# Optimization experiments

Measured on AMD Instinct MI355X. Metric: run time of the kernel, lower is better.

## Reference

```python
import jax, jax.numpy as jnp
from jax import lax
import numpy as np

COST_CLASS, COST_BOX, COST_GIOU = 1.0, 5.0, 2.0
B, Q, C, T = 16, 900, 92, 100
INF = jnp.float32(1e18)


def setup_inputs() -> dict:
    key = jax.random.key(0)
    k1, k2, k3, k4 = jax.random.split(key, 4)
    pred_logits = jax.random.normal(k1, (B, Q, C), jnp.float32)

    def mk_boxes(k, n):
        kc, ks = jax.random.split(k)
        cxcy = jax.random.uniform(kc, (B, n, 2), jnp.float32) * 0.8 + 0.1
        wh = jax.random.uniform(ks, (B, n, 2), jnp.float32) * 0.2 + 0.05
        return jnp.concatenate([cxcy, wh], axis=-1)  # valid cxcywh in (0,1)

    pred_boxes = mk_boxes(k2, Q)
    tgt_boxes = mk_boxes(k3, T)
    tgt_labels = jax.random.randint(k4, (B, T), 0, C)
    return {"pred_logits": pred_logits, "pred_boxes": pred_boxes,
            "tgt_labels": tgt_labels, "tgt_boxes": tgt_boxes}


def box_cxcywh_to_xyxy(b):
    cx, cy, w, h = b[..., 0], b[..., 1], b[..., 2], b[..., 3]
    return jnp.stack([cx - 0.5 * w, cy - 0.5 * h, cx + 0.5 * w, cy + 0.5 * h], axis=-1)


def generalized_box_iou(a, b):
    # a: [B,Q,4] xyxy, b: [B,T,4] xyxy -> [B,Q,T]
    area_a = (a[..., 2] - a[..., 0]) * (a[..., 3] - a[..., 1])  # [B,Q]
    area_b = (b[..., 2] - b[..., 0]) * (b[..., 3] - b[..., 1])  # [B,T]
    a_ = a[:, :, None, :]
    b_ = b[:, None, :, :]
    lt = jnp.maximum(a_[..., :2], b_[..., :2])
    rb = jnp.minimum(a_[..., 2:], b_[..., 2:])
    wh = jnp.clip(rb - lt, 0.0)
    inter = wh[..., 0] * wh[..., 1]
    union = area_a[:, :, None] + area_b[:, None, :] - inter
    iou = inter / union
    lt_c = jnp.minimum(a_[..., :2], b_[..., :2])
    rb_c = jnp.maximum(a_[..., 2:], b_[..., 2:])
    wh_c = jnp.clip(rb_c - lt_c, 0.0)
    area_c = wh_c[..., 0] * wh_c[..., 1]
    return iou - (area_c - union) / area_c


def cost_matrix(pred_logits, pred_boxes, tgt_labels, tgt_boxes):
    probs = jax.nn.softmax(pred_logits, axis=-1)                         # [B,Q,C]
    cost_class = -jnp.take_along_axis(probs, tgt_labels[:, None, :], 2)  # [B,Q,T]
    cost_box = jnp.abs(pred_boxes[:, :, None, :] - tgt_boxes[:, None, :, :]).sum(-1)
    cost_giou = -generalized_box_iou(box_cxcywh_to_xyxy(pred_boxes),
                                     box_cxcywh_to_xyxy(tgt_boxes))
    return COST_BOX * cost_box + COST_CLASS * cost_class + COST_GIOU * cost_giou


def hungarian(cost):
    # Jonker-Volgenant shortest augmenting path. cost: [n, m], n <= m, minimize.
    # Returns col_for_row [n]: column assigned to each row.
    n, m = cost.shape

    def solve_row(i, uvp):
        u, v, p = uvp  # u:[n+1] row potentials, v:[m+1] col potentials, p:[m+1] col->row (n = free)
        p = p.at[m].set(i)  # virtual start column holds current row
        minv = jnp.full((m,), INF, jnp.float32)
        way = jnp.zeros((m,), jnp.int32)
        used = jnp.zeros((m + 1,), bool)
        j0 = jnp.int32(m)

        def cond(s):
            _, _, _, _, _, j0 = s
            return p[j0] != n  # stop when a free column is reached

        def body(s):
            u, v, minv, way, used, j0 = s
            used = used.at[j0].set(True)
            i0 = p[j0]
            cur = cost[i0] - u[i0] - v[:m]           # reduced costs of row i0
            mask = (~used[:m]) & (cur < minv)
            minv = jnp.where(mask, cur, minv)
            way = jnp.where(mask, j0, way)
            mvals = jnp.where(used[:m], INF, minv)
            j1 = jnp.argmin(mvals).astype(jnp.int32)
            delta = mvals[j1]
            u = u.at[p].add(jnp.where(used, delta, 0.0))
            v = v - jnp.where(used, delta, 0.0)
            minv = jnp.where(used[:m], minv, minv - delta)
            return (u, v, minv, way, used, j1)

        u, v, minv, way, used, j0 = lax.while_loop(cond, body, (u, v, minv, way, used, j0))

        def acond(s):
            _, j0 = s
            return j0 != m

        def abody(s):
            p, j0 = s
            j1 = way[j0]
            p = p.at[j0].set(p[j1])
            return (p, j1)

        p, _ = lax.while_loop(acond, abody, (p, j0))
        return (u, v, p)

    u0 = jnp.zeros((n + 1,), jnp.float32)
    v0 = jnp.zeros((m + 1,), jnp.float32)
    p0 = jnp.full((m + 1,), n, jnp.int32)
    _, _, p = lax.fori_loop(0, n, solve_row, (u0, v0, p0))
    col_for_row = jnp.zeros((n + 1,), jnp.int32).at[p[:m]].set(
        jnp.arange(m, dtype=jnp.int32))[:n]
    return col_for_row


def reference(pred_logits, pred_boxes, tgt_labels, tgt_boxes):
    cost = cost_matrix(pred_logits, pred_boxes, tgt_labels, tgt_boxes)  # [B,Q,T]
    # assign each target (row) to a distinct query (col); vmap over batch
    q_per_t = jax.vmap(hungarian)(jnp.swapaxes(cost, 1, 2))  # [B,T]
    order = jnp.argsort(q_per_t, axis=-1)                    # sort by query idx (scipy convention)
    q_idx = jnp.take_along_axis(q_per_t, order, axis=-1)     # query indices  [B,T]
    t_idx = order.astype(jnp.int32)                          # target indices [B,T]
    return cost, q_idx, t_idx
```

## Files before the change

### kernel.cpp

```cpp
#include <hip/hip_runtime.h>

#define BB 16
#define QQ 900
#define QP 960
#define VIRT QP
#define CC 92
#define TT 100
#define INFF 1e18f
#define NK 15

#define DPP_STEP_F(x, ctrl, OP)                                             \
  do {                                                                      \
    float _o = __int_as_float(__builtin_amdgcn_update_dpp(                  \
        __float_as_int(x), __float_as_int(x), (ctrl), 0xF, 0xF, false));    \
    (x) = OP((x), _o);                                                      \
  } while (0)

__device__ __forceinline__ float wave_fmax63(float x) {
  DPP_STEP_F(x, 0xB1, fmaxf);
  DPP_STEP_F(x, 0x4E, fmaxf);
  DPP_STEP_F(x, 0x141, fmaxf);
  DPP_STEP_F(x, 0x140, fmaxf);
  DPP_STEP_F(x, 0x142, fmaxf);
  DPP_STEP_F(x, 0x143, fmaxf);
  return x;
}
__device__ __forceinline__ float wave_fmin63(float x) {
  DPP_STEP_F(x, 0xB1, fminf);
  DPP_STEP_F(x, 0x4E, fminf);
  DPP_STEP_F(x, 0x141, fminf);
  DPP_STEP_F(x, 0x140, fminf);
  DPP_STEP_F(x, 0x142, fminf);
  DPP_STEP_F(x, 0x143, fminf);
  return x;
}
__device__ __forceinline__ float wave_fadd63(float x) {
#define ADDF(a, b) ((a) + (b))
  DPP_STEP_F(x, 0xB1, ADDF);
  DPP_STEP_F(x, 0x4E, ADDF);
  DPP_STEP_F(x, 0x141, ADDF);
  DPP_STEP_F(x, 0x140, ADDF);
  DPP_STEP_F(x, 0x142, ADDF);
  DPP_STEP_F(x, 0x143, ADDF);
#undef ADDF
  return x;
}
__device__ __forceinline__ int wave_imin63(int x) {
  {int _o=__builtin_amdgcn_update_dpp(x,x,0xB1,0xF,0xF,false); x=_o<x?_o:x;}
  {int _o=__builtin_amdgcn_update_dpp(x,x,0x4E,0xF,0xF,false); x=_o<x?_o:x;}
  {int _o=__builtin_amdgcn_update_dpp(x,x,0x141,0xF,0xF,false);x=_o<x?_o:x;}
  {int _o=__builtin_amdgcn_update_dpp(x,x,0x140,0xF,0xF,false);x=_o<x?_o:x;}
  {int _o=__builtin_amdgcn_update_dpp(x,x,0x142,0xF,0xF,false);x=_o<x?_o:x;}
  {int _o=__builtin_amdgcn_update_dpp(x,x,0x143,0xF,0xF,false);x=_o<x?_o:x;}
  return x;
}

__device__ __forceinline__ int p_get(unsigned a, unsigned b, unsigned c,
                                     unsigned d, int j) {
  const int l = j & 63, kq = j >> 6;
  unsigned r0 = (unsigned)__builtin_amdgcn_readlane((int)a, l);
  unsigned r1 = (unsigned)__builtin_amdgcn_readlane((int)b, l);
  unsigned r2 = (unsigned)__builtin_amdgcn_readlane((int)c, l);
  unsigned r3 = (unsigned)__builtin_amdgcn_readlane((int)d, l);
  unsigned r = (kq < 8) ? (kq < 4 ? r0 : r1) : (kq < 12 ? r2 : r3);
  return (int)((r >> ((kq & 3) * 8)) & 0xFFu);
}

#define P_SET(jj, val)                                                      \
  do {                                                                      \
    const int _j = (jj); const int _kq = _j >> 6;                           \
    const unsigned _sh = (unsigned)((_kq & 3) * 8);                         \
    const unsigned _nm = ~(0xFFu << _sh);                                   \
    const unsigned _in = ((unsigned)(val) & 0xFFu) << _sh;                  \
    const bool _own = (lane == (_j & 63));                                  \
    if (_kq < 4)       { if (_own) p4a = (p4a & _nm) | _in; }               \
    else if (_kq < 8)  { if (_own) p4b = (p4b & _nm) | _in; }               \
    else if (_kq < 12) { if (_own) p4c = (p4c & _nm) | _in; }               \
    else               { if (_own) p4d = (p4d & _nm) | _in; }               \
  } while (0)

__global__ __launch_bounds__(64) void cost_kernel(
    const float* __restrict__ logits,
    const float* __restrict__ pboxes,
    const int*   __restrict__ tlabels,
    const float* __restrict__ tboxes,
    float* __restrict__ cost,
    float* __restrict__ costT,
    int ctp)
{
  const int bq   = blockIdx.x;
  const int b    = bq / QQ;
  const int q    = bq - b * QQ;
  const int lane = threadIdx.x;

  __shared__ float sl[CC];

  const float a = logits[(size_t)bq * CC + lane];
  const float bb2 = (lane < CC - 64)
                        ? logits[(size_t)bq * CC + 64 + lane]
                        : -3.402823466e38f;

  float mx = fmaxf(a, bb2);
  mx = wave_fmax63(mx);
  const float m = __int_as_float(
      __builtin_amdgcn_readlane(__float_as_int(mx), 63));

  const float e0 = expf(a - m);
  const float e1 = (lane < CC - 64) ? expf(bb2 - m) : 0.0f;
  sl[lane] = e0;
  if (lane < CC - 64) sl[64 + lane] = e1;

  float sm = e0 + e1;
  sm = wave_fadd63(sm);
  const float ssum = __int_as_float(
      __builtin_amdgcn_readlane(__float_as_int(sm), 63));

  const float4 pbv = ((const float4*)pboxes)[bq];
  const float pax1 = pbv.x - 0.5f * pbv.z, pay1 = pbv.y - 0.5f * pbv.w;
  const float pax2 = pbv.x + 0.5f * pbv.z, pay2 = pbv.y + 0.5f * pbv.w;
  const float area_a = (pax2 - pax1) * (pay2 - pay1);

  for (int t = lane; t < TT; t += 64) {
    const int lab = tlabels[b * TT + t];
    const float cc = -(sl[lab] / ssum);

    const float4 tb = ((const float4*)tboxes)[b * TT + t];
    const float cbox = fabsf(pbv.x - tb.x) + fabsf(pbv.y - tb.y) +
                       fabsf(pbv.z - tb.z) + fabsf(pbv.w - tb.w);

    const float bx1 = tb.x - 0.5f * tb.z, by1 = tb.y - 0.5f * tb.w;
    const float bx2 = tb.x + 0.5f * tb.z, by2 = tb.y + 0.5f * tb.w;
    const float area_b = (bx2 - bx1) * (by2 - by1);

    const float ltx = fmaxf(pax1, bx1), lty = fmaxf(pay1, by1);
    const float rbx = fminf(pax2, bx2), rby = fminf(pay2, by2);
    const float iw = fmaxf(rbx - ltx, 0.0f), ih = fmaxf(rby - lty, 0.0f);
    const float inter = iw * ih;
    const float uni = area_a + area_b - inter;
    const float iou = inter / uni;

    const float cx1 = fminf(pax1, bx1), cy1 = fminf(pay1, by1);
    const float cx2 = fmaxf(pax2, bx2), cy2 = fmaxf(pay2, by2);
    const float cw = fmaxf(cx2 - cx1, 0.0f), ch = fmaxf(cy2 - cy1, 0.0f);
    const float ac = cw * ch;
    const float giou = iou - (ac - uni) / ac;

    const float cval = 5.0f * cbox + cc - 2.0f * giou;
    cost[(size_t)bq * TT + t] = cval;
    if (ctp) costT[((size_t)b * TT + t) * ctp + q] = cval;
  }
  if (ctp == QP && q < QP - QQ) {
    for (int t = lane; t < TT; t += 64)
      costT[((size_t)b * TT + t) * QP + QQ + q] = INFF;
  }
}

__global__ void __launch_bounds__(64)
hungarianT_kernel(
    const float* __restrict__ ct,
    float* __restrict__ out_q,
    float* __restrict__ out_t)
{
  const int b    = blockIdx.x;
  const int lane = threadIdx.x;

  __shared__ int way_lds[QP];
  __shared__ int qpt[TT];

  const float* __restrict__ base = ct + (size_t)b * TT * QP;

#pragma unroll
  for (int k = 0; k < NK; ++k) way_lds[k * 64 + lane] = -1;

  unsigned p4a = 0x64646464u, p4b = 0x64646464u;
  unsigned p4c = 0x64646464u, p4d = 0x64646464u;

  float u0 = 0.0f, u1 = 0.0f;
  float v[NK];
#pragma unroll
  for (int k = 0; k < NK; ++k) v[k] = 0.0f;

  float c[NK];
#pragma unroll
  for (int k = 0; k < NK; ++k) c[k] = base[k * 64 + lane];

  for (int i = 0; i < TT; ++i) {
    float minv[NK];
#pragma unroll
    for (int k = 0; k < NK; ++k) minv[k] = INFF;
    unsigned umask = 0;
    const int stamp = i << 12;

    int i0 = i;
    int j0 = VIRT;
    int jfin;

    float us = (i0 < 64) ? u0 : u1;
    float ui0 = __int_as_float(
        __builtin_amdgcn_readlane(__float_as_int(us), i0 & 63));

    for (int step = 0; step < 128; ++step) {
      const bool first = (j0 == VIRT);
      if (i0 == lane)      umask |= (1u << 30);
      if (i0 == 64 + lane) umask |= (1u << 31);
      if (!first && (j0 & 63) == lane) umask |= (1u << (j0 >> 6));

      float lmin  = INFF;
      int   kbest = 0;
#pragma unroll
      for (int k = 0; k < NK; ++k) {
        const bool  uk  = (umask >> k) & 1u;
        const float cur = c[k] - ui0 - v[k];
        const bool  imp = !uk && (cur < minv[k]);
        if (imp) {
          minv[k] = cur;
          if (!first) way_lds[k * 64 + lane] = stamp | j0;
        }
        const float eff = uk ? INFF : minv[k];
        if (eff < lmin) { lmin = eff; kbest = k; }
      }
      const int lidx = (kbest << 6) + lane;

      if (first && i + 1 < TT) {
        const float* __restrict__ nrow = base + (size_t)(i + 1) * QP;
#pragma unroll
        for (int k = 0; k < NK; ++k) c[k] = nrow[k * 64 + lane];
      }

      float red = wave_fmin63(lmin);
      const float delta = __int_as_float(
          __builtin_amdgcn_readlane(__float_as_int(red), 63));
      const unsigned long long bmask = __ballot(lmin == delta);
      const int wl = (int)(__ffsll((long long)bmask) - 1);
      const int j1 = __builtin_amdgcn_readlane(lidx, wl);

      const int  i0n = p_get(p4a, p4b, p4c, p4d, j1);
      const bool fin = (i0n == TT);

      if (!fin) {
        const float* __restrict__ prow = base + (size_t)i0n * QP;
#pragma unroll
        for (int k = 0; k < NK; ++k) c[k] = prow[k * 64 + lane];
      }

      u0 += ((umask >> 30) & 1u) ? delta : 0.0f;
      u1 += (umask >> 31)        ? delta : 0.0f;
#pragma unroll
      for (int k = 0; k < NK; ++k)
        v[k] -= ((umask >> k) & 1u) ? delta : 0.0f;
      if (!fin) {
#pragma unroll
        for (int k = 0; k < NK; ++k)
          minv[k] -= ((umask >> k) & 1u) ? 0.0f : delta;
      }
      asm volatile("" ::: "memory");

      if (fin) { jfin = j1; break; }
      float us2 = (i0n < 64) ? u0 : u1;
      ui0 = __int_as_float(
          __builtin_amdgcn_readlane(__float_as_int(us2), i0n & 63));
      j0 = j1;
      i0 = i0n;
    }

    const bool single = (j0 == VIRT);

    if (!single && i + 1 < TT) {
      const float* __restrict__ nrow = base + (size_t)(i + 1) * QP;
#pragma unroll
      for (int k = 0; k < NK; ++k) c[k] = nrow[k * 64 + lane];
    }

    if (single) {
      P_SET(jfin, i);
    } else {
      int j = jfin;
      for (int hop = 0; hop < 128 && j != VIRT; ++hop) {
        int raw = way_lds[j];
        raw = __builtin_amdgcn_readfirstlane(raw);
        const int jn = ((raw >> 12) == i) ? (raw & 0xFFF) : VIRT;
        const int pj = (jn == VIRT) ? i : p_get(p4a, p4b, p4c, p4d, jn);
        P_SET(j, pj);
        j = jn;
      }
    }
    asm volatile("" ::: "memory");
  }

#pragma unroll
  for (int k = 0; k < NK; ++k) {
    const unsigned reg = (k < 4) ? p4a : (k < 8) ? p4b : (k < 12) ? p4c : p4d;
    const int r = (int)((reg >> ((k & 3) * 8)) & 0xFFu);
    const int j = k * 64 + lane;
    if (r < TT) qpt[r] = j;
  }
  __syncthreads();

  for (int t = lane; t < TT; t += 64) {
    const int myq = qpt[t];
    int rank = 0;
    for (int t2 = 0; t2 < TT; ++t2) rank += (qpt[t2] < myq) ? 1 : 0;
    out_q[b * TT + rank] = (float)myq;
    out_t[b * TT + rank] = (float)t;
  }
}

__global__ void __launch_bounds__(64)
hungarian_kernel(
    const float* __restrict__ cost,
    const float* __restrict__ costT,
    float* __restrict__ out_q,
    float* __restrict__ out_t)
{
  const int b    = blockIdx.x;
  const int lane = threadIdx.x;

  __shared__ int p_lds[QQ + 1];
  __shared__ int way_lds[QQ];
  __shared__ int qpt[TT];

  const float* base;
  size_t rs, cs;
  if (costT) { base = costT + (size_t)b * TT * QQ; rs = QQ; cs = 1; }
  else       { base = cost  + (size_t)b * QQ * TT; rs = 1;  cs = TT; }

  for (int j = lane; j <= QQ; j += 64) p_lds[j] = TT;

  float u0 = 0.0f, u1 = 0.0f;
  float v[NK];
#pragma unroll
  for (int k = 0; k < NK; ++k) v[k] = 0.0f;

  float c[NK];
#pragma unroll
  for (int k = 0; k < NK; ++k) {
    const int j = k * 64 + lane;
    c[k] = (j < QQ) ? base[(size_t)j * cs] : 0.0f;
  }

  for (int i = 0; i < TT; ++i) {
    p_lds[QQ] = i;

    float minv[NK];
#pragma unroll
    for (int k = 0; k < NK; ++k) minv[k] = INFF;
    unsigned umask = 0;
    bool t0 = false, t1 = false;

    int i0 = i;
    int j0 = QQ;
    int jfin;

    float us = (i0 < 64) ? u0 : u1;
    float ui0 = __int_as_float(
        __builtin_amdgcn_readlane(__float_as_int(us), i0 & 63));

    while (true) {
      t0 = t0 || (i0 == lane);
      t1 = t1 || (i0 == 64 + lane);
      if (j0 != QQ) {
        if ((j0 & 63) == lane) umask |= (1u << (j0 >> 6));
      }

      float lmin = INFF;
      int   lidx = QQ;
#pragma unroll
      for (int k = 0; k < NK; ++k) {
        const int j = k * 64 + lane;
        if (j < QQ && !((umask >> k) & 1u)) {
          const float cur = c[k] - ui0 - v[k];
          if (cur < minv[k]) { minv[k] = cur; way_lds[j] = j0; }
          if (minv[k] < lmin) { lmin = minv[k]; lidx = j; }
        }
      }

      float red = wave_fmin63(lmin);
      const float delta = __int_as_float(
          __builtin_amdgcn_readlane(__float_as_int(red), 63));
      int cand = (lmin == delta) ? lidx : 0x7FFFFFFF;
      int redi = wave_imin63(cand);
      const int j1 = __builtin_amdgcn_readlane(redi, 63);

      int i0n = p_lds[j1];
      i0n = __builtin_amdgcn_readfirstlane(i0n);
      const bool fin = (i0n == TT);

      u0 += t0 ? delta : 0.0f;
      u1 += t1 ? delta : 0.0f;
#pragma unroll
      for (int k = 0; k < NK; ++k) {
        const bool uk = (umask >> k) & 1u;
        v[k]    -= uk ? delta : 0.0f;
        minv[k] -= uk ? 0.0f  : delta;
      }

      if (!fin) {
        float us2 = (i0n < 64) ? u0 : u1;
        ui0 = __int_as_float(
            __builtin_amdgcn_readlane(__float_as_int(us2), i0n & 63));
#pragma unroll
        for (int k = 0; k < NK; ++k) {
          const int j = k * 64 + lane;
          if (j < QQ) c[k] = base[(size_t)i0n * rs + (size_t)j * cs];
        }
      }
      asm volatile("" ::: "memory");

      if (fin) { jfin = j1; break; }
      j0 = j1;
      i0 = i0n;
    }

    if (i + 1 < TT) {
#pragma unroll
      for (int k = 0; k < NK; ++k) {
        const int jj = k * 64 + lane;
        if (jj < QQ) c[k] = base[(size_t)(i + 1) * rs + (size_t)jj * cs];
      }
    }

    int j = jfin;
    while (j != QQ) {
      const int jn = way_lds[j];
      const int pj = p_lds[jn];
      p_lds[j] = pj;
      j = jn;
    }
    asm volatile("" ::: "memory");
  }

#pragma unroll
  for (int k = 0; k < NK; ++k) {
    const int j = k * 64 + lane;
    if (j < QQ) {
      const int r = p_lds[j];
      if (r < TT) qpt[r] = j;
    }
  }
  __syncthreads();

  for (int t = lane; t < TT; t += 64) {
    const int myq = qpt[t];
    int rank = 0;
    for (int t2 = 0; t2 < TT; ++t2) rank += (qpt[t2] < myq) ? 1 : 0;
    out_q[b * TT + rank] = (float)myq;
    out_t[b * TT + rank] = (float)t;
  }
}

extern "C" void kernel_launch(void* const* d_in, const int* in_sizes, int n_in,
                              void* d_out, int out_size, void* d_ws, size_t ws_size,
                              hipStream_t stream) {
  const float* logits  = (const float*)d_in[0];
  const float* pboxes  = (const float*)d_in[1];
  const int*   tlabels = (const int*)d_in[2];
  const float* tboxes  = (const float*)d_in[3];

  float* out  = (float*)d_out;
  float* cost = out;
  float* oq   = out + (size_t)BB * QQ * TT;
  float* ot   = oq + (size_t)BB * TT;

  const size_t padded_bytes = (size_t)BB * TT * QP * sizeof(float);
  const size_t plain_bytes  = (size_t)BB * TT * QQ * sizeof(float);

  if (ws_size >= padded_bytes) {
    float* costT = (float*)d_ws;
    hipLaunchKernelGGL(cost_kernel, dim3(BB * QQ), dim3(64), 0, stream,
                       logits, pboxes, tlabels, tboxes, cost, costT, QP);
    hipLaunchKernelGGL(hungarianT_kernel, dim3(BB), dim3(64), 0, stream,
                       costT, oq, ot);
  } else if (ws_size >= plain_bytes) {
    float* costT = (float*)d_ws;
    hipLaunchKernelGGL(cost_kernel, dim3(BB * QQ), dim3(64), 0, stream,
                       logits, pboxes, tlabels, tboxes, cost, costT, QQ);
    hipLaunchKernelGGL(hungarian_kernel, dim3(BB), dim3(64), 0, stream,
                       cost, costT, oq, ot);
  } else {
    hipLaunchKernelGGL(cost_kernel, dim3(BB * QQ), dim3(64), 0, stream,
                       logits, pboxes, tlabels, tboxes, cost, (float*)nullptr, 0);
    hipLaunchKernelGGL(hungarian_kernel, dim3(BB), dim3(64), 0, stream,
                       cost, (const float*)nullptr, oq, ot);
  }
}
```

Baseline: 200.2 us.

## Batch single-step Hungarian rows speculatively, fall back on first column collision

Restructures the Hungarian solver into epochs. Each epoch precomputes each remaining row's minimum reduced-cost column without data dependencies, so row loads can be prefetched. It then commits rows in order whose chosen column is still free, and falls back to the full augmenting-path search only at the first collision. This is meant to cut the serial dependent-step latency for the many rows that augment in one step. The cost is that rows after a collision are recomputed in later epochs, which could do extra work when collisions happen early and often.

Result: slower. 247.8 us (+23.8%).

```diff
diff --git a/kernel.cpp b/kernel.cpp
--- a/kernel.cpp
+++ b/kernel.cpp
@@ -53,6 +53,10 @@
   {int _o=__builtin_amdgcn_update_dpp(x,x,0x142,0xF,0xF,false);x=_o<x?_o:x;}
   {int _o=__builtin_amdgcn_update_dpp(x,x,0x143,0xF,0xF,false);x=_o<x?_o:x;}
   return x;
+}
+
+__device__ __forceinline__ float readlane_f(float x, int l) {
+  return __int_as_float(__builtin_amdgcn_readlane(__float_as_int(x), l));
 }
 
 __device__ __forceinline__ int p_get(unsigned a, unsigned b, unsigned c,
@@ -102,8 +106,7 @@
 
   float mx = fmaxf(a, bb2);
   mx = wave_fmax63(mx);
-  const float m = __int_as_float(
-      __builtin_amdgcn_readlane(__float_as_int(mx), 63));
+  const float m = readlane_f(mx, 63);
 
   const float e0 = expf(a - m);
   const float e1 = (lane < CC - 64) ? expf(bb2 - m) : 0.0f;
@@ -112,8 +115,7 @@
 
   float sm = e0 + e1;
   sm = wave_fadd63(sm);
-  const float ssum = __int_as_float(
-      __builtin_amdgcn_readlane(__float_as_int(sm), 63));
+  const float ssum = readlane_f(sm, 63);
 
   const float4 pbv = ((const float4*)pboxes)[bq];
   const float pax1 = pbv.x - 0.5f * pbv.z, pay1 = pbv.y - 0.5f * pbv.w;
@@ -180,111 +182,149 @@
 #pragma unroll
   for (int k = 0; k < NK; ++k) v[k] = 0.0f;
 
-  float c[NK];
-#pragma unroll
-  for (int k = 0; k < NK; ++k) c[k] = base[k * 64 + lane];
-
-  for (int i = 0; i < TT; ++i) {
-    float minv[NK];
-#pragma unroll
-    for (int k = 0; k < NK; ++k) minv[k] = INFF;
-    unsigned umask = 0;
-    const int stamp = i << 12;
-
-    int i0 = i;
-    int j0 = VIRT;
-    int jfin;
-
-    float us = (i0 < 64) ? u0 : u1;
-    float ui0 = __int_as_float(
-        __builtin_amdgcn_readlane(__float_as_int(us), i0 & 63));
-
-    for (int step = 0; step < 128; ++step) {
-      const bool first = (j0 == VIRT);
-      if (i0 == lane)      umask |= (1u << 30);
-      if (i0 == 64 + lane) umask |= (1u << 31);
-      if (!first && (j0 & 63) == lane) umask |= (1u << (j0 >> 6));
-
+  int rbase = 0;
+  for (int epoch = 0; epoch <= TT && rbase < TT; ++epoch) {
+    float valv0 = 0.0f, valv1 = 0.0f;
+    int   colv0 = 0,    colv1 = 0;
+
+    float cn[NK];
+    {
+      const float* __restrict__ rp = base + (size_t)rbase * QP;
+#pragma unroll
+      for (int k = 0; k < NK; ++k) cn[k] = rp[k * 64 + lane];
+    }
+    for (int s = rbase; s < TT; ++s) {
+      float cc[NK];
+#pragma unroll
+      for (int k = 0; k < NK; ++k) cc[k] = cn[k];
+      if (s + 1 < TT) {
+        const float* __restrict__ rp = base + (size_t)(s + 1) * QP;
+#pragma unroll
+        for (int k = 0; k < NK; ++k) cn[k] = rp[k * 64 + lane];
+      }
       float lmin  = INFF;
       int   kbest = 0;
 #pragma unroll
       for (int k = 0; k < NK; ++k) {
-        const bool  uk  = (umask >> k) & 1u;
-        const float cur = c[k] - ui0 - v[k];
-        const bool  imp = !uk && (cur < minv[k]);
-        if (imp) {
-          minv[k] = cur;
-          if (!first) way_lds[k * 64 + lane] = stamp | j0;
+        const float cur = cc[k] - v[k];
+        if (cur < lmin) { lmin = cur; kbest = k; }
+      }
+      const int lidx = (kbest << 6) + lane;
+      float red = wave_fmin63(lmin);
+      const float delta = readlane_f(red, 63);
+      const unsigned long long bm = __ballot(lmin == delta);
+      const int wl = (int)(__ffsll((long long)bm) - 1);
+      const int j1 = __builtin_amdgcn_readlane(lidx, wl);
+      const int off = s - rbase;
+      if (off < 64) { if (lane == off)      { valv0 = delta; colv0 = j1; } }
+      else          { if (lane == off - 64) { valv1 = delta; colv1 = j1; } }
+    }
+
+    int sfb = -1;
+    for (int s = rbase; s < TT; ++s) {
+      const int off = s - rbase;
+      float sv; int sc;
+      if (off < 64) { sv = readlane_f(valv0, off);      sc = __builtin_amdgcn_readlane(colv0, off); }
+      else          { sv = readlane_f(valv1, off - 64); sc = __builtin_amdgcn_readlane(colv1, off - 64); }
+      const int pm = p_get(p4a, p4b, p4c, p4d, sc);
+      if (pm != TT) { sfb = s; break; }
+      P_SET(sc, s);
+      u0 = (lane == s)      ? sv : u0;
+      u1 = (lane == s - 64) ? sv : u1;
+    }
+    if (sfb < 0) { rbase = TT; break; }
+
+    {
+      const int s = sfb;
+      float c2[NK];
+      {
+        const float* __restrict__ rp = base + (size_t)s * QP;
+#pragma unroll
+        for (int k = 0; k < NK; ++k) c2[k] = rp[k * 64 + lane];
+      }
+      float minv[NK];
+#pragma unroll
+      for (int k = 0; k < NK; ++k) minv[k] = INFF;
+      unsigned umask = 0;
+      const int stamp = s << 12;
+
+      int i0 = s;
+      int j0 = VIRT;
+      int jfin;
+
+      float us_ = (i0 < 64) ? u0 : u1;
+      float ui0 = readlane_f(us_, i0 & 63);
+
+      for (int step = 0; step < 256; ++step) {
+        const bool first = (j0 == VIRT);
+        if (i0 == lane)      umask |= (1u << 30);
+        if (i0 == 64 + lane) umask |= (1u << 31);
+        if (!first && (j0 & 63) == lane) umask |= (1u << (j0 >> 6));
+
+        float lmin  = INFF;
+        int   kbest = 0;
+#pragma unroll
+        for (int k = 0; k < NK; ++k) {
+          const bool  uk  = (umask >> k) & 1u;
+          const float cur = c2[k] - ui0 - v[k];
+          const bool  imp = !uk && (cur < minv[k]);
+          if (imp) {
+            minv[k] = cur;
+            if (!first) way_lds[k * 64 + lane] = stamp | j0;
+          }
+          const float eff = uk ? INFF : minv[k];
+          if (eff < lmin) { lmin = eff; kbest = k; }
         }
-        const float eff = uk ? INFF : minv[k];
-        if (eff < lmin) { lmin = eff; kbest = k; }
-      }
-      const int lidx = (kbest << 6) + lane;
-
-      if (first && i + 1 < TT) {
-        const float* __restrict__ nrow = base + (size_t)(i + 1) * QP;
-#pragma unroll
-        for (int k = 0; k < NK; ++k) c[k] = nrow[k * 64 + lane];
-      }
-
-      float red = wave_fmin63(lmin);
-      const float delta = __int_as_float(
-          __builtin_amdgcn_readlane(__float_as_int(red), 63));
-      const unsigned long long bmask = __ballot(lmin == delta);
-      const int wl = (int)(__ffsll((long long)bmask) - 1);
-      const int j1 = __builtin_amdgcn_readlane(lidx, wl);
-
-      const int  i0n = p_get(p4a, p4b, p4c, p4d, j1);
-      const bool fin = (i0n == TT);
-
-      if (!fin) {
-        const float* __restrict__ prow = base + (size_t)i0n * QP;
-#pragma unroll
-        for (int k = 0; k < NK; ++k) c[k] = prow[k * 64 + lane];
-      }
-
-      u0 += ((umask >> 30) & 1u) ? delta : 0.0f;
-      u1 += (umask >> 31)        ? delta : 0.0f;
-#pragma unroll
-      for (int k = 0; k < NK; ++k)
-        v[k] -= ((umask >> k) & 1u) ? delta : 0.0f;
-      if (!fin) {
+        const int lidx = (kbest << 6) + lane;
+
+        float red = wave_fmin63(lmin);
+        const float delta = readlane_f(red, 63);
+        const unsigned long long bm = __ballot(lmin == delta);
+        const int wl = (int)(__ffsll((long long)bm) - 1);
+        const int j1 = __builtin_amdgcn_readlane(lidx, wl);
+
+        const int  i0n = p_get(p4a, p4b, p4c, p4d, j1);
+        const bool fin = (i0n == TT);
+
+        if (!fin) {
+          const float* __restrict__ prow = base + (size_t)i0n * QP;
+#pragma unroll
+          for (int k = 0; k < NK; ++k) c2[k] = prow[k * 64 + lane];
+        }
+
+        u0 += ((umask >> 30) & 1u) ? delta : 0.0f;
+        u1 += (umask >> 31)        ? delta : 0.0f;
 #pragma unroll
         for (int k = 0; k < NK; ++k)
-          minv[k] -= ((umask >> k) & 1u) ? 0.0f : delta;
-      }
-      asm volatile("" ::: "memory");
-
-      if (fin) { jfin = j1; break; }
-      float us2 = (i0n < 64) ? u0 : u1;
-      ui0 = __int_as_float(
-          __builtin_amdgcn_readlane(__float_as_int(us2), i0n & 63));
-      j0 = j1;
-      i0 = i0n;
-    }
-
-    const bool single = (j0 == VIRT);
-
-    if (!single && i + 1 < TT) {
-      const float* __restrict__ nrow = base + (size_t)(i + 1) * QP;
-#pragma unroll
-      for (int k = 0; k < NK; ++k) c[k] = nrow[k * 64 + lane];
-    }
-
-    if (single) {
-      P_SET(jfin, i);
-    } else {
-      int j = jfin;
-      for (int hop = 0; hop < 128 && j != VIRT; ++hop) {
-        int raw = way_lds[j];
-        raw = __builtin_amdgcn_readfirstlane(raw);
-        const int jn = ((raw >> 12) == i) ? (raw & 0xFFF) : VIRT;
-        const int pj = (jn == VIRT) ? i : p_get(p4a, p4b, p4c, p4d, jn);
-        P_SET(j, pj);
-        j = jn;
-      }
-    }
-    asm volatile("" ::: "memory");
+          v[k] -= ((umask >> k) & 1u) ? delta : 0.0f;
+        if (!fin) {
+#pragma unroll
+          for (int k = 0; k < NK; ++k)
+            minv[k] -= ((umask >> k) & 1u) ? 0.0f : delta;
+        }
+
+        if (fin) { jfin = j1; break; }
+        float us2 = (i0n < 64) ? u0 : u1;
+        ui0 = readlane_f(us2, i0n & 63);
+        j0 = j1;
+        i0 = i0n;
+      }
+
+      if (j0 == VIRT) {
+        P_SET(jfin, s);
+      } else {
+        int j = jfin;
+        for (int hop = 0; hop < 256 && j != VIRT; ++hop) {
+          int raw = way_lds[j];
+          raw = __builtin_amdgcn_readfirstlane(raw);
+          const int jn = ((raw >> 12) == s) ? (raw & 0xFFF) : VIRT;
+          const int pj = (jn == VIRT) ? s : p_get(p4a, p4b, p4c, p4d, jn);
+          P_SET(j, pj);
+          j = jn;
+        }
+      }
+    }
+    rbase = sfb + 1;
   }
 
 #pragma unroll
@@ -352,8 +392,7 @@
     int jfin;
 
     float us = (i0 < 64) ? u0 : u1;
-    float ui0 = __int_as_float(
-        __builtin_amdgcn_readlane(__float_as_int(us), i0 & 63));
+    float ui0 = readlane_f(us, i0 & 63);
 
     while (true) {
       t0 = t0 || (i0 == lane);
@@ -375,8 +414,7 @@
       }
 
       float red = wave_fmin63(lmin);
-      const float delta = __int_as_float(
-          __builtin_amdgcn_readlane(__float_as_int(red), 63));
+      const float delta = readlane_f(red, 63);
       int cand = (lmin == delta) ? lidx : 0x7FFFFFFF;
       int redi = wave_imin63(cand);
       const int j1 = __builtin_amdgcn_readlane(redi, 63);
@@ -396,8 +434,7 @@
 
       if (!fin) {
         float us2 = (i0n < 64) ? u0 : u1;
-        ui0 = __int_as_float(
-            __builtin_amdgcn_readlane(__float_as_int(us2), i0n & 63));
+        ui0 = readlane_f(us2, i0n & 63);
 #pragma unroll
         for (int k = 0; k < NK; ++k) {
           const int j = k * 64 + lane;
```

## Stage cost rows into LDS via global_load_lds with double-buffered prefetch

Applied to the files above, without the earlier changes.

The Hungarian kernel now copies cost rows into a double-buffered LDS row buffer with direct global-to-LDS loads, instead of holding them in registers. The next row is prefetched while the current row is processed. A per-column bitmask replaces the p_get lookup for the finish check, and ui0 is taken as zero for the start row, since u of a newly added row is assumed to be zero. The aim is to cut register pressure and overlap row loads with compute, at the cost of an explicit full vmcnt wait on every augmenting step and an LDS read for every column in each step.

New measurement: 235.4 us. +17.6%, slower.

```diff
diff --git a/kernel.cpp b/kernel.cpp
--- a/kernel.cpp
+++ b/kernel.cpp
@@ -53,6 +53,22 @@
   {int _o=__builtin_amdgcn_update_dpp(x,x,0x142,0xF,0xF,false);x=_o<x?_o:x;}
   {int _o=__builtin_amdgcn_update_dpp(x,x,0x143,0xF,0xF,false);x=_o<x?_o:x;}
   return x;
+}
+
+__device__ __forceinline__ float readlane_f(float x, int l) {
+  return __int_as_float(__builtin_amdgcn_readlane(__float_as_int(x), l));
+}
+
+__device__ __forceinline__ void stage_row(const float* __restrict__ row,
+                                          float* buf, int lane) {
+  typedef __attribute__((address_space(1))) const void gv_t;
+  typedef __attribute__((address_space(3))) void lv_t;
+  __builtin_amdgcn_global_load_lds((gv_t*)(row + lane * 4),       (lv_t*)(buf),       16, 0, 0);
+  __builtin_amdgcn_global_load_lds((gv_t*)(row + 256 + lane * 4), (lv_t*)(buf + 256), 16, 0, 0);
+  __builtin_amdgcn_global_load_lds((gv_t*)(row + 512 + lane * 4), (lv_t*)(buf + 512), 16, 0, 0);
+  __builtin_amdgcn_global_load_lds((gv_t*)(row + 768 + lane),     (lv_t*)(buf + 768), 4, 0, 0);
+  __builtin_amdgcn_global_load_lds((gv_t*)(row + 832 + lane),     (lv_t*)(buf + 832), 4, 0, 0);
+  __builtin_amdgcn_global_load_lds((gv_t*)(row + 896 + lane),     (lv_t*)(buf + 896), 4, 0, 0);
 }
 
 __device__ __forceinline__ int p_get(unsigned a, unsigned b, unsigned c,
@@ -102,8 +118,7 @@
 
   float mx = fmaxf(a, bb2);
   mx = wave_fmax63(mx);
-  const float m = __int_as_float(
-      __builtin_amdgcn_readlane(__float_as_int(mx), 63));
+  const float m = readlane_f(mx, 63);
 
   const float e0 = expf(a - m);
   const float e1 = (lane < CC - 64) ? expf(bb2 - m) : 0.0f;
@@ -112,8 +127,7 @@
 
   float sm = e0 + e1;
   sm = wave_fadd63(sm);
-  const float ssum = __int_as_float(
-      __builtin_amdgcn_readlane(__float_as_int(sm), 63));
+  const float ssum = readlane_f(sm, 63);
 
   const float4 pbv = ((const float4*)pboxes)[bq];
   const float pax1 = pbv.x - 0.5f * pbv.z, pay1 = pbv.y - 0.5f * pbv.w;
@@ -164,6 +178,7 @@
   const int b    = blockIdx.x;
   const int lane = threadIdx.x;
 
+  __shared__ __align__(16) float rowbuf[2][QP];
   __shared__ int way_lds[QP];
   __shared__ int qpt[TT];
 
@@ -174,17 +189,22 @@
 
   unsigned p4a = 0x64646464u, p4b = 0x64646464u;
   unsigned p4c = 0x64646464u, p4d = 0x64646464u;
+  unsigned cmask = 0;
 
   float u0 = 0.0f, u1 = 0.0f;
   float v[NK];
 #pragma unroll
   for (int k = 0; k < NK; ++k) v[k] = 0.0f;
 
-  float c[NK];
-#pragma unroll
-  for (int k = 0; k < NK; ++k) c[k] = base[k * 64 + lane];
+  stage_row(base, &rowbuf[0][0], lane);
 
   for (int i = 0; i < TT; ++i) {
+    float* bufc = &rowbuf[i & 1][0];
+
+    asm volatile("s_waitcnt vmcnt(0)" ::: "memory");
+    if (i + 1 < TT)
+      stage_row(base + (size_t)(i + 1) * QP, &rowbuf[(i + 1) & 1][0], lane);
+
     float minv[NK];
 #pragma unroll
     for (int k = 0; k < NK; ++k) minv[k] = INFF;
@@ -194,12 +214,9 @@
     int i0 = i;
     int j0 = VIRT;
     int jfin;
-
-    float us = (i0 < 64) ? u0 : u1;
-    float ui0 = __int_as_float(
-        __builtin_amdgcn_readlane(__float_as_int(us), i0 & 63));
-
-    for (int step = 0; step < 128; ++step) {
+    float ui0 = 0.0f;
+
+    for (int step = 0; step < 256; ++step) {
       const bool first = (j0 == VIRT);
       if (i0 == lane)      umask |= (1u << 30);
       if (i0 == 64 + lane) umask |= (1u << 31);
@@ -209,8 +226,9 @@
       int   kbest = 0;
 #pragma unroll
       for (int k = 0; k < NK; ++k) {
+        const float ck  = bufc[k * 64 + lane];
         const bool  uk  = (umask >> k) & 1u;
-        const float cur = c[k] - ui0 - v[k];
+        const float cur = ck - ui0 - v[k];
         const bool  imp = !uk && (cur < minv[k]);
         if (imp) {
           minv[k] = cur;
@@ -221,61 +239,55 @@
       }
       const int lidx = (kbest << 6) + lane;
 
-      if (first && i + 1 < TT) {
-        const float* __restrict__ nrow = base + (size_t)(i + 1) * QP;
-#pragma unroll
-        for (int k = 0; k < NK; ++k) c[k] = nrow[k * 64 + lane];
-      }
-
       float red = wave_fmin63(lmin);
-      const float delta = __int_as_float(
-          __builtin_amdgcn_readlane(__float_as_int(red), 63));
-      const unsigned long long bmask = __ballot(lmin == delta);
-      const int wl = (int)(__ffsll((long long)bmask) - 1);
+      const float delta = readlane_f(red, 63);
+      const unsigned long long bm = __ballot(lmin == delta);
+      const int wl = (int)(__ffsll((long long)bm) - 1);
       const int j1 = __builtin_amdgcn_readlane(lidx, wl);
 
-      const int  i0n = p_get(p4a, p4b, p4c, p4d, j1);
-      const bool fin = (i0n == TT);
-
-      if (!fin) {
-        const float* __restrict__ prow = base + (size_t)i0n * QP;
-#pragma unroll
-        for (int k = 0; k < NK; ++k) c[k] = prow[k * 64 + lane];
-      }
-
+      const unsigned cmw =
+          (unsigned)__builtin_amdgcn_readlane((int)cmask, j1 & 63);
+      const bool fin = !((cmw >> (j1 >> 6)) & 1u);
+
+      if (fin) {
+        jfin = j1;
+        u0 += ((umask >> 30) & 1u) ? delta : 0.0f;
+        u1 += (umask >> 31)        ? delta : 0.0f;
+        if (!first) {
+#pragma unroll
+          for (int k = 0; k < NK; ++k)
+            v[k] -= ((umask >> k) & 1u) ? delta : 0.0f;
+        }
+        break;
+      }
+
+      const int i0n = p_get(p4a, p4b, p4c, p4d, j1);
       u0 += ((umask >> 30) & 1u) ? delta : 0.0f;
       u1 += (umask >> 31)        ? delta : 0.0f;
 #pragma unroll
-      for (int k = 0; k < NK; ++k)
-        v[k] -= ((umask >> k) & 1u) ? delta : 0.0f;
-      if (!fin) {
-#pragma unroll
-        for (int k = 0; k < NK; ++k)
-          minv[k] -= ((umask >> k) & 1u) ? 0.0f : delta;
-      }
-      asm volatile("" ::: "memory");
-
-      if (fin) { jfin = j1; break; }
-      float us2 = (i0n < 64) ? u0 : u1;
-      ui0 = __int_as_float(
-          __builtin_amdgcn_readlane(__float_as_int(us2), i0n & 63));
+      for (int k = 0; k < NK; ++k) {
+        const bool uk = (umask >> k) & 1u;
+        v[k]    -= uk ? delta : 0.0f;
+        minv[k] -= uk ? 0.0f  : delta;
+      }
+      {
+        float us2 = (i0n < 64) ? u0 : u1;
+        ui0 = readlane_f(us2, i0n & 63);
+      }
+      asm volatile("s_waitcnt lgkmcnt(0)" ::: "memory");
+      stage_row(base + (size_t)i0n * QP, bufc, lane);
+      asm volatile("s_waitcnt vmcnt(0)" ::: "memory");
       j0 = j1;
       i0 = i0n;
     }
 
-    const bool single = (j0 == VIRT);
-
-    if (!single && i + 1 < TT) {
-      const float* __restrict__ nrow = base + (size_t)(i + 1) * QP;
-#pragma unroll
-      for (int k = 0; k < NK; ++k) c[k] = nrow[k * 64 + lane];
-    }
-
-    if (single) {
+    if (lane == (jfin & 63)) cmask |= (1u << (jfin >> 6));
+
+    if (j0 == VIRT) {
       P_SET(jfin, i);
     } else {
       int j = jfin;
-      for (int hop = 0; hop < 128 && j != VIRT; ++hop) {
+      for (int hop = 0; hop < 256 && j != VIRT; ++hop) {
         int raw = way_lds[j];
         raw = __builtin_amdgcn_readfirstlane(raw);
         const int jn = ((raw >> 12) == i) ? (raw & 0xFFF) : VIRT;
@@ -284,7 +296,6 @@
         j = jn;
       }
     }
-    asm volatile("" ::: "memory");
   }
 
 #pragma unroll
@@ -352,8 +363,7 @@
     int jfin;
 
     float us = (i0 < 64) ? u0 : u1;
-    float ui0 = __int_as_float(
-        __builtin_amdgcn_readlane(__float_as_int(us), i0 & 63));
+    float ui0 = readlane_f(us, i0 & 63);
 
     while (true) {
       t0 = t0 || (i0 == lane);
@@ -375,8 +385,7 @@
       }
 
       float red = wave_fmin63(lmin);
-      const float delta = __int_as_float(
-          __builtin_amdgcn_readlane(__float_as_int(red), 63));
+      const float delta = readlane_f(red, 63);
       int cand = (lmin == delta) ? lidx : 0x7FFFFFFF;
       int redi = wave_imin63(cand);
       const int j1 = __builtin_amdgcn_readlane(redi, 63);
@@ -396,8 +405,7 @@
 
       if (!fin) {
         float us2 = (i0n < 64) ? u0 : u1;
-        ui0 = __int_as_float(
-            __builtin_amdgcn_readlane(__float_as_int(us2), i0n & 63));
+        ui0 = readlane_f(us2, i0n & 63);
 #pragma unroll
         for (int k = 0; k < NK; ++k) {
           const int j = k * 64 + lane;
```
